# Kernel optimization log

Measured on AMD Instinct MI355X. Metric: run time of the kernel, lower is better.

Reference implementation:

```python
import jax, jax.numpy as jnp
import numpy as np

S = 2048        # sequence length
D_MODEL = 1024  # model dim
H = 16          # mqa_n_queries
D = 64          # mqa_query_dim
WIN = 128       # mqa_window


def setup_inputs() -> dict:
    key = jax.random.key(0)
    ks = jax.random.split(key, 5)
    scale_in = 1.0 / np.sqrt(D_MODEL)
    return {
        "x": jax.random.normal(ks[0], (S, D_MODEL), dtype=jnp.float32),
        "Wqkv": jax.random.normal(ks[1], (D * (H + 2), D_MODEL), dtype=jnp.float32) * scale_in,
        "bqkv": jax.random.normal(ks[2], (D * (H + 2),), dtype=jnp.float32) * 0.01,
        "Wout": jax.random.normal(ks[3], (D_MODEL, D_MODEL), dtype=jnp.float32) * scale_in,
        "bout": jax.random.normal(ks[4], (D_MODEL,), dtype=jnp.float32) * 0.01,
    }


def reference(x, Wqkv, bqkv, Wout, bout):
    seq = x.shape[0]
    # fused QKV projection: 1 shared K, 1 shared V, H query heads (MQA)
    qkv = x @ Wqkv.T + bqkv                        # (S, D*(H+2))
    k = qkv[:, :D]                                 # (S, D) shared key
    v = qkv[:, D:2 * D]                            # (S, D) shared value
    q = qkv[:, 2 * D:].reshape(seq, H, D)          # (S, H, D)

    i = jnp.arange(seq)[:, None]
    j = jnp.arange(seq)[None, :]
    mask = (j <= i) & (j > i - WIN)                # (S, S)

    # NOTE: original multiplies by sqrt(D) (not 1/sqrt(D)); kept faithful.
    scores = jnp.sqrt(jnp.float32(D)) * jnp.einsum('ihd,jd->hij', q, k)  # (H, S, S)
    scores = jnp.where(mask, scores, -jnp.inf)
    attn = jax.nn.softmax(scores, axis=-1)         # every row has >=1 valid entry

    o = jnp.einsum('hij,jd->ihd', attn, v).reshape(seq, H * D)  # (S, d_model)
    return o @ Wout.T + bout
```

## Files before the change

### kernel.cpp

```cpp
#include <hip/hip_runtime.h>
#include <math.h>

#define S_LEN 2048
#define DMODEL 1024
#define NHEAD 16
#define DHEAD 64
#define WIN 128
#define NQKV 1152

typedef _Float16 f16x8 __attribute__((ext_vector_type(8)));
typedef float f32x4 __attribute__((ext_vector_type(4)));

__device__ __forceinline__ ushort f2h(float f) {
  union { _Float16 h; ushort u; } v; v.h = (_Float16)f; return v.u;
}

typedef __attribute__((address_space(1))) const unsigned GU;
typedef __attribute__((address_space(3))) unsigned LU;
__device__ __forceinline__ void async16(const ushort* g, ushort* l) {
  __builtin_amdgcn_global_load_lds((GU*)g, (LU*)l, 16, 0, 0);
}

__global__ __launch_bounds__(256)
void convert_kernel(const float4* __restrict__ x, const float4* __restrict__ wq,
                    const float4* __restrict__ wo,
                    ushort4* __restrict__ x16, ushort4* __restrict__ w16,
                    ushort4* __restrict__ wo16) {
  const int NX4 = (S_LEN * DMODEL) / 4;
  const int NW4 = (NQKV * DMODEL) / 4;
  const int NO4 = (DMODEL * DMODEL) / 4;
  const int i = blockIdx.x * 256 + threadIdx.x;
  if (i < NX4) {
    const float4 v = x[i];
    ushort4 h; h.x = f2h(v.x); h.y = f2h(v.y); h.z = f2h(v.z); h.w = f2h(v.w);
    x16[i] = h;
  } else if (i < NX4 + NW4) {
    const int j = i - NX4;
    const float s = ((j >> 8) >= 2 * DHEAD) ? 8.0f : 1.0f;
    const float4 v = wq[j];
    ushort4 h; h.x = f2h(v.x * s); h.y = f2h(v.y * s); h.z = f2h(v.z * s); h.w = f2h(v.w * s);
    w16[j] = h;
  } else {
    const int j = i - NX4 - NW4;
    if (j < NO4) {
      const float4 v = wo[j];
      ushort4 h; h.x = f2h(v.x); h.y = f2h(v.y); h.z = f2h(v.z); h.w = f2h(v.w);
      wo16[j] = h;
    }
  }
}

template<int MODE>
__global__ __launch_bounds__(256)
void gemm32(const ushort* __restrict__ A, const ushort* __restrict__ B,
            const float* __restrict__ bias, float* __restrict__ Cout,
            ushort* __restrict__ k16, ushort* __restrict__ vT, ushort* __restrict__ q16,
            int M, int N, int K) {
  __shared__ __align__(16) ushort sA[2][32 * 64];
  __shared__ __align__(16) ushort sB[2][64 * 64];
  const int t = threadIdx.x;
  const int w = t >> 6, lane = t & 63;
  const int quad = lane >> 4, l16 = lane & 15;
  const int wn = w * 16;
  const int m0 = blockIdx.x * 32, n0 = blockIdx.y * 64;

  const int lr = lane >> 3;
  const int lc = (lane & 7) ^ lr;
  const size_t aBase = (size_t)(m0 + 8 * w + lr) * K + lc * 8;
  const size_t bBase = (size_t)(n0 + 16 * w + lr) * K + lc * 8;

  f32x4 acc[2] = {};

  auto STAGE = [&](int ktile, int b) {
    const size_t koff = (size_t)ktile << 6;
    async16(A + aBase + koff, &sA[b][(8 * w) * 64]);
#pragma unroll
    for (int i = 0; i < 2; ++i)
      async16(B + bBase + (size_t)(8 * i) * K + koff, &sB[b][(16 * w + 8 * i) * 64]);
  };

  STAGE(0, 0);
  __syncthreads();

  const int NT = K >> 6;
  for (int kt = 0; kt < NT; ++kt) {
    const int cur = kt & 1;
    if (kt + 1 < NT) STAGE(kt + 1, cur ^ 1);

    f16x8 af[2][2], bf[2];
#pragma unroll
    for (int kst = 0; kst < 2; ++kst) {
      const int cp = ((kst << 2) | quad) ^ (l16 & 7);
#pragma unroll
      for (int i = 0; i < 2; ++i)
        af[kst][i] = *(const f16x8*)(&sA[cur][(16 * i + l16) * 64 + cp * 8]);
      bf[kst] = *(const f16x8*)(&sB[cur][(wn + l16) * 64 + cp * 8]);
    }
#pragma unroll
    for (int kst = 0; kst < 2; ++kst)
#pragma unroll
      for (int i = 0; i < 2; ++i)
        acc[i] = __builtin_amdgcn_mfma_f32_16x16x32_f16(af[kst][i], bf[kst], acc[i], 0, 0, 0);
    __syncthreads();
  }

  const int cb = n0 + wn;
  const int col = cb + l16;
#pragma unroll
  for (int i = 0; i < 2; ++i) {
    if (MODE == 0) {
      const float b = bias[col];
#pragma unroll
      for (int r = 0; r < 4; ++r) {
        const int row = m0 + 16 * i + quad * 4 + r;
        Cout[(size_t)row * N + col] = acc[i][r] + b;
      }
    } else {
      const float bscale = (cb >= 2 * DHEAD) ? 8.0f : 1.0f;
      const float b = bias[col] * bscale;
#pragma unroll
      for (int r = 0; r < 4; ++r) {
        const int row = m0 + 16 * i + quad * 4 + r;
        const ushort h = f2h(acc[i][r] + b);
        if (cb >= 2 * DHEAD) {
          q16[(size_t)row * DMODEL + (col - 2 * DHEAD)] = h;
        } else if (cb < DHEAD) {
          k16[(size_t)row * DHEAD + col] = h;
        } else {
          vT[(size_t)(col - DHEAD) * S_LEN + row] = h;
        }
      }
    }
  }
}

#define QT 4
#define NTK 10
#define KST 5
#define PSTR 176

__global__ __launch_bounds__(256)
void attn_kernel(const ushort* __restrict__ k16, const ushort* __restrict__ vT,
                 const ushort* __restrict__ q16, ushort* __restrict__ obuf) {
  __shared__ __align__(16) ushort lds[64 * PSTR + 64 * PSTR];
  ushort* Ksw = lds;
  ushort* P   = lds;
  ushort* Vt  = lds + 64 * PSTR;

  const int t = threadIdx.x;
  const int i0 = blockIdx.x * QT;
  const int jbase = (i0 >= WIN - 1) ? ((i0 - (WIN - 1)) & ~7) : 0;
  const int w = t >> 6, lane = t & 63;
  const int quad = lane >> 4, l16 = lane & 15;
  const int qg = i0 + w;

#pragma unroll
  for (int i = 0; i < 5; ++i) {
    const int n = 5 * w + i;
    const int r = 8 * n + (lane >> 3);
    const int cs = (lane & 7) ^ (r & 7);
    async16(k16 + (size_t)(jbase + r) * DHEAD + cs * 8, &Ksw[n * 512]);
  }
  {
    const int d = t >> 2, p = t & 3;
#pragma unroll
    for (int it = 0; it < 5; ++it) {
      const int c = p + 4 * it;
      const uint4 raw = *(const uint4*)(vT + (size_t)d * S_LEN + jbase + c * 8);
      *(uint4*)(&Vt[d * PSTR + c * 8]) = raw;
    }
  }
  f16x8 qf[2];
  {
    const size_t qbase = (size_t)qg * DMODEL + l16 * DHEAD;
#pragma unroll
    for (int kst = 0; kst < 2; ++kst)
      qf[kst] = *(const f16x8*)(q16 + qbase + kst * 32 + quad * 8);
  }
  __syncthreads();

  f32x4 acc[NTK] = {};
#pragma unroll
  for (int nt = 0; nt < NTK; ++nt) {
#pragma unroll
    for (int kst = 0; kst < 2; ++kst) {
      const int cp = ((kst << 2) | quad) ^ (l16 & 7);
      const f16x8 bf = *(const f16x8*)(&Ksw[(nt * 16 + l16) * 64 + cp * 8]);
      acc[nt] = __builtin_amdgcn_mfma_f32_16x16x32_f16(qf[kst], bf, acc[nt], 0, 0, 0);
    }
  }
  __syncthreads();

  float inv_l[4];
#pragma unroll
  for (int nt = 0; nt < NTK; ++nt) {
    const int jg = jbase + nt * 16 + l16;
    const bool valid = (jg <= qg) && (jg > qg - WIN);
#pragma unroll
    for (int r = 0; r < 4; ++r)
      if (!valid) acc[nt][r] = -1e30f;
  }
#pragma unroll
  for (int r = 0; r < 4; ++r) {
    float m = acc[0][r];
#pragma unroll
    for (int nt = 1; nt < NTK; ++nt) m = fmaxf(m, acc[nt][r]);
#pragma unroll
    for (int off = 1; off < 16; off <<= 1) m = fmaxf(m, __shfl_xor(m, off));
    float s = 0.f;
#pragma unroll
    for (int nt = 0; nt < NTK; ++nt) {
      const float e = __expf(acc[nt][r] - m);
      acc[nt][r] = e;
      s += e;
    }
#pragma unroll
    for (int off = 1; off < 16; off <<= 1) s += __shfl_xor(s, off);
    inv_l[r] = 1.0f / s;
  }
  {
    const int mrow0 = w * 16 + quad * 4;
#pragma unroll
    for (int r = 0; r < 4; ++r)
#pragma unroll
      for (int nt = 0; nt < NTK; ++nt)
        P[(mrow0 + r) * PSTR + nt * 16 + l16] = f2h(acc[nt][r]);
  }
  __syncthreads();

  f32x4 o[4] = {};
#pragma unroll
  for (int kst = 0; kst < KST; ++kst) {
    const f16x8 a = *(const f16x8*)(&P[(w * 16 + l16) * PSTR + kst * 32 + quad * 8]);
#pragma unroll
    for (int nd = 0; nd < 4; ++nd) {
      const f16x8 b = *(const f16x8*)(&Vt[(nd * 16 + l16) * PSTR + kst * 32 + quad * 8]);
      o[nd] = __builtin_amdgcn_mfma_f32_16x16x32_f16(a, b, o[nd], 0, 0, 0);
    }
  }

  {
    const size_t obase = (size_t)qg * DMODEL;
#pragma unroll
    for (int nd = 0; nd < 4; ++nd)
#pragma unroll
      for (int r = 0; r < 4; ++r) {
        const int col = (quad * 4 + r) * DHEAD + nd * 16 + l16;
        obuf[obase + col] = f2h(o[nd][r] * inv_l[r]);
      }
  }
}

extern "C" void kernel_launch(void* const* d_in, const int* in_sizes, int n_in,
                              void* d_out, int out_size, void* d_ws, size_t ws_size,
                              hipStream_t stream) {
  const float* x    = (const float*)d_in[0];
  const float* Wqkv = (const float*)d_in[1];
  const float* bqkv = (const float*)d_in[2];
  const float* Wout = (const float*)d_in[3];
  const float* bout = (const float*)d_in[4];
  float* out = (float*)d_out;

  char* w = (char*)d_ws;
  ushort* x16  = (ushort*)(w + 0);
  ushort* w16  = (ushort*)(w + 4194304);
  ushort* wo16 = (ushort*)(w + 6553600);
  ushort* k16  = (ushort*)(w + 8650752);
  ushort* vT   = (ushort*)(w + 8921088);
  ushort* q16  = (ushort*)(w + 9191424);
  ushort* obuf = (ushort*)(w + 13385728);

  convert_kernel<<<4224, 256, 0, stream>>>(
      (const float4*)x, (const float4*)Wqkv, (const float4*)Wout,
      (ushort4*)x16, (ushort4*)w16, (ushort4*)wo16);

  dim3 g1(S_LEN / 32, NQKV / 64);
  gemm32<1><<<g1, 256, 0, stream>>>(x16, w16, bqkv, nullptr, k16, vT, q16,
                                    S_LEN, NQKV, DMODEL);

  attn_kernel<<<S_LEN / QT, 256, 0, stream>>>(k16, vT, q16, obuf);

  dim3 g2(S_LEN / 32, DMODEL / 64);
  gemm32<0><<<g2, 256, 0, stream>>>(obuf, wo16, bout, out, nullptr, nullptr, nullptr,
                                    S_LEN, DMODEL, DMODEL);
}
```

Before: 105.4 us.

## Triple-buffer GEMM K tiles and load attention V fragments directly to registers

The GEMM moves from a double-buffered to a triple-buffered LDS pipeline. It prefetches two tiles ahead and uses an explicit vmcnt wait plus one barrier per iteration instead of two __syncthreads. The attention kernel drops the V staging through LDS and loads the V^T fragments straight from global memory into registers, which halves LDS use and removes a barrier. This adds register pressure (20 f16x8 V fragments per lane) and relies on the per-wave P rows being written and read by the same wave without a block barrier.

```diff
diff --git a/kernel.cpp b/kernel.cpp
--- a/kernel.cpp
+++ b/kernel.cpp
@@ -56,8 +56,8 @@
             const float* __restrict__ bias, float* __restrict__ Cout,
             ushort* __restrict__ k16, ushort* __restrict__ vT, ushort* __restrict__ q16,
             int M, int N, int K) {
-  __shared__ __align__(16) ushort sA[2][32 * 64];
-  __shared__ __align__(16) ushort sB[2][64 * 64];
+  __shared__ __align__(16) ushort sA[3][32 * 64];
+  __shared__ __align__(16) ushort sB[3][64 * 64];
   const int t = threadIdx.x;
   const int w = t >> 6, lane = t & 63;
   const int quad = lane >> 4, l16 = lane & 15;
@@ -80,12 +80,19 @@
   };
 
   STAGE(0, 0);
-  __syncthreads();
+  STAGE(1, 1);
 
   const int NT = K >> 6;
+  int c0 = 0, c1 = 1, c2 = 2;
   for (int kt = 0; kt < NT; ++kt) {
-    const int cur = kt & 1;
-    if (kt + 1 < NT) STAGE(kt + 1, cur ^ 1);
+    if (kt + 1 < NT) {
+      asm volatile("s_waitcnt vmcnt(3)" ::: "memory");
+    } else {
+      asm volatile("s_waitcnt vmcnt(0)" ::: "memory");
+    }
+    __builtin_amdgcn_s_barrier();
+    __builtin_amdgcn_sched_barrier(0);
+    if (kt + 2 < NT) STAGE(kt + 2, c2);
 
     f16x8 af[2][2], bf[2];
 #pragma unroll
@@ -93,15 +100,16 @@
       const int cp = ((kst << 2) | quad) ^ (l16 & 7);
 #pragma unroll
       for (int i = 0; i < 2; ++i)
-        af[kst][i] = *(const f16x8*)(&sA[cur][(16 * i + l16) * 64 + cp * 8]);
-      bf[kst] = *(const f16x8*)(&sB[cur][(wn + l16) * 64 + cp * 8]);
+        af[kst][i] = *(const f16x8*)(&sA[c0][(16 * i + l16) * 64 + cp * 8]);
+      bf[kst] = *(const f16x8*)(&sB[c0][(wn + l16) * 64 + cp * 8]);
     }
 #pragma unroll
     for (int kst = 0; kst < 2; ++kst)
 #pragma unroll
       for (int i = 0; i < 2; ++i)
         acc[i] = __builtin_amdgcn_mfma_f32_16x16x32_f16(af[kst][i], bf[kst], acc[i], 0, 0, 0);
-    __syncthreads();
+
+    const int tmp = c0; c0 = c1; c1 = c2; c2 = tmp;
   }
 
   const int cb = n0 + wn;
@@ -142,10 +150,9 @@
 __global__ __launch_bounds__(256)
 void attn_kernel(const ushort* __restrict__ k16, const ushort* __restrict__ vT,
                  const ushort* __restrict__ q16, ushort* __restrict__ obuf) {
-  __shared__ __align__(16) ushort lds[64 * PSTR + 64 * PSTR];
+  __shared__ __align__(16) ushort lds[64 * PSTR];
   ushort* Ksw = lds;
   ushort* P   = lds;
-  ushort* Vt  = lds + 64 * PSTR;
 
   const int t = threadIdx.x;
   const int i0 = blockIdx.x * QT;
@@ -161,15 +168,6 @@
     const int cs = (lane & 7) ^ (r & 7);
     async16(k16 + (size_t)(jbase + r) * DHEAD + cs * 8, &Ksw[n * 512]);
   }
-  {
-    const int d = t >> 2, p = t & 3;
-#pragma unroll
-    for (int it = 0; it < 5; ++it) {
-      const int c = p + 4 * it;
-      const uint4 raw = *(const uint4*)(vT + (size_t)d * S_LEN + jbase + c * 8);
-      *(uint4*)(&Vt[d * PSTR + c * 8]) = raw;
-    }
-  }
   f16x8 qf[2];
   {
     const size_t qbase = (size_t)qg * DMODEL + l16 * DHEAD;
@@ -178,6 +176,14 @@
       qf[kst] = *(const f16x8*)(q16 + qbase + kst * 32 + quad * 8);
   }
   __syncthreads();
+
+  f16x8 vb[KST][4];
+#pragma unroll
+  for (int kst = 0; kst < KST; ++kst)
+#pragma unroll
+    for (int nd = 0; nd < 4; ++nd)
+      vb[kst][nd] = *(const f16x8*)(vT + (size_t)(nd * 16 + l16) * S_LEN +
+                                    jbase + kst * 32 + quad * 8);
 
   f32x4 acc[NTK] = {};
 #pragma unroll
@@ -226,17 +232,14 @@
       for (int nt = 0; nt < NTK; ++nt)
         P[(mrow0 + r) * PSTR + nt * 16 + l16] = f2h(acc[nt][r]);
   }
-  __syncthreads();
 
   f32x4 o[4] = {};
 #pragma unroll
   for (int kst = 0; kst < KST; ++kst) {
     const f16x8 a = *(const f16x8*)(&P[(w * 16 + l16) * PSTR + kst * 32 + quad * 8]);
 #pragma unroll
-    for (int nd = 0; nd < 4; ++nd) {
-      const f16x8 b = *(const f16x8*)(&Vt[(nd * 16 + l16) * PSTR + kst * 32 + quad * 8]);
-      o[nd] = __builtin_amdgcn_mfma_f32_16x16x32_f16(a, b, o[nd], 0, 0, 0);
-    }
+    for (int nd = 0; nd < 4; ++nd)
+      o[nd] = __builtin_amdgcn_mfma_f32_16x16x32_f16(a, vb[kst][nd], o[nd], 0, 0, 0);
   }
 
   {
```

Result: slower. 113.7 us (+7.9%).
